# Performance work log

Measured on AMD Instinct MI355X. Metric: run time of the kernel, lower is better.

## Reference

```python
import jax, jax.numpy as jnp
import numpy as np

SEQ, BATCH, IN, HID, LAYERS, TAPE = 256, 128, 512, 512, 2, 30


def setup_inputs() -> dict:
    key = jax.random.key(0)
    ks = jax.random.split(key, 10)
    s = 0.05  # small init scale for numerical stability of tanh/softmax
    return {
        "xs": jax.random.normal(ks[0], (SEQ, BATCH, IN), jnp.float32),
        # stacked per-layer LSTM params (layer-1 input dim == HID == IN)
        "W_ih": jax.random.normal(ks[1], (LAYERS, 4 * HID, IN), jnp.float32) * s,
        "W_hh": jax.random.normal(ks[2], (LAYERS, 4 * HID, HID), jnp.float32) * s,
        "b_ih": jax.random.normal(ks[3], (LAYERS, 4 * HID), jnp.float32) * s,
        "b_hh": jax.random.normal(ks[4], (LAYERS, 4 * HID), jnp.float32) * s,
        "attn_wh": jax.random.normal(ks[5], (LAYERS, HID, HID), jnp.float32) * s,
        "attn_wx": jax.random.normal(ks[6], (LAYERS, HID, IN), jnp.float32) * s,
        "attn_wht": jax.random.normal(ks[7], (LAYERS, HID, HID), jnp.float32) * s,
        "attn_v": jax.random.normal(ks[8], (LAYERS, HID), jnp.float32) * s,
    }


def reference(xs, W_ih, W_hh, b_ih, b_hh, attn_wh, attn_wx, attn_wht, attn_v):
    L, B, H = W_ih.shape[0], xs.shape[1], W_hh.shape[-1]

    def lstm_step(x, h, c):
        # x: (B, IN); h, c: (L, B, H). PyTorch gate order: i, f, g, o.
        inp = x
        hs, cs = [], []
        for l in range(L):
            gates = inp @ W_ih[l].T + b_ih[l] + h[l] @ W_hh[l].T + b_hh[l]
            i_, f_, g_, o_ = jnp.split(gates, 4, axis=-1)
            c_new = jax.nn.sigmoid(f_) * c[l] + jax.nn.sigmoid(i_) * jnp.tanh(g_)
            h_new = jax.nn.sigmoid(o_) * jnp.tanh(c_new)
            hs.append(h_new)
            cs.append(c_new)
            inp = h_new
        return jnp.stack(hs), jnp.stack(cs)

    zeros = jnp.zeros((L, B, H), xs.dtype)
    # First TAPE steps: source never updates prev_hidden/cell inside the fill
    # loop, so every step starts from zero state -> vmap over time.
    h_tape0, c_tape0 = jax.vmap(lambda x: lstm_step(x, zeros, zeros))(xs[:TAPE])

    # einsums 'jll,...' / 'ijj,...' contract nothing: they take diagonals.
    wh_diag = jnp.diagonal(attn_wh, axis1=1, axis2=2)    # (L, H)
    wht_diag = jnp.diagonal(attn_wht, axis1=1, axis2=2)  # (L, H)

    def step(carry, x):
        h_tape, c_tape, prev_h = carry
        hidden_attn = h_tape * wh_diag[:, None, :]            # (T, L, B, H)
        x_attn = jnp.einsum('lhi,bi->lbh', attn_wx, x)        # (L, B, H)
        ht_attn = prev_h * wht_diag[:, None, :]               # (L, B, H)
        a = jnp.tanh(hidden_attn + x_attn + ht_attn)          # (T, L, B, H)
        score = jnp.einsum('tlbh,lh->tlb', a, attn_v)         # (T, L, B)
        alpha = jax.nn.softmax(score, axis=0)
        prev_h_new = jnp.einsum('tlb,tlbh->lbh', alpha, h_tape)
        prev_c_new = jnp.einsum('tlb,tlbh->lbh', alpha, c_tape)
        h_new, c_new = lstm_step(x, prev_h_new, prev_c_new)
        h_tape = jnp.concatenate([h_tape[1:], h_new[None]], axis=0)
        c_tape = jnp.concatenate([c_tape[1:], c_new[None]], axis=0)
        return (h_tape, c_tape, prev_h_new), None

    (h_tape, _, _), _ = jax.lax.scan(step, (h_tape0, c_tape0, zeros), xs[TAPE:])
    return h_tape[:, -1]  # (TAPE, B, H): last layer across the tape
```

## Files before the change

kernel.cpp:

```cpp
#include <hip/hip_runtime.h>
#include <hip/hip_fp16.h>

typedef _Float16 f16;
typedef _Float16 half8 __attribute__((ext_vector_type(8)));
typedef _Float16 half4v __attribute__((ext_vector_type(4)));
typedef float floatx4 __attribute__((ext_vector_type(4)));
typedef unsigned long long u64;

#define SEQ   256
#define BATCH 128
#define HID   512
#define NL    2
#define TAPE  30
#define NG    2048
#define NBLK  256

__device__ __forceinline__ float fsig(float x)  { return 1.f/(1.f+__expf(-x)); }
__device__ __forceinline__ float ftanh(float x) { return 1.f - 2.f/(1.f+__expf(2.f*x)); }

__device__ __forceinline__ void ast64(void* p, u64 v){
    __hip_atomic_store((u64*)p, v, __ATOMIC_RELAXED, __HIP_MEMORY_SCOPE_AGENT);
}
__device__ __forceinline__ void ast32(void* p, unsigned v){
    __hip_atomic_store((unsigned*)p, v, __ATOMIC_RELAXED, __HIP_MEMORY_SCOPE_AGENT);
}
__device__ __forceinline__ unsigned packh2(float a, float b){
    union { f16 h[2]; unsigned u; } c; c.h[0]=(f16)a; c.h[1]=(f16)b; return c.u;
}
__device__ __forceinline__ float2 unpackh2(unsigned u){
    union { unsigned u; f16 h[2]; } c; c.u=u;
    float2 r; r.x=(float)c.h[0]; r.y=(float)c.h[1]; return r;
}

#define BAR_ROOT 512
#define BAR_REL  544
__device__ __forceinline__ void gridbar(unsigned* bar, unsigned gen){
    __syncthreads();
    if (threadIdx.x == 0){
        unsigned* leaf = bar + ((blockIdx.x >> 4) << 5);
        bool releaser = false;
        unsigned p = __hip_atomic_fetch_add(leaf, 1u, __ATOMIC_RELAXED, __HIP_MEMORY_SCOPE_AGENT);
        if ((p & 15u) == 15u){
            unsigned q = __hip_atomic_fetch_add(bar + BAR_ROOT, 1u, __ATOMIC_RELAXED, __HIP_MEMORY_SCOPE_AGENT);
            if ((q & 15u) == 15u){
                __hip_atomic_store(bar + BAR_REL, gen, __ATOMIC_RELAXED, __HIP_MEMORY_SCOPE_AGENT);
                releaser = true;
            }
        }
        if (!releaser){
            while (__hip_atomic_load(bar + BAR_REL, __ATOMIC_RELAXED, __HIP_MEMORY_SCOPE_AGENT) < gen){
                __builtin_amdgcn_s_sleep(8);
            }
        }
        __builtin_amdgcn_fence(__ATOMIC_ACQUIRE, "agent");
    }
    __syncthreads();
}

__global__ void k_setup_w(const float* __restrict__ W_ih, const float* __restrict__ W_hh,
                          const float* __restrict__ b_ih, const float* __restrict__ b_hh,
                          f16* __restrict__ Wcat, float* __restrict__ bsum)
{
    int idx = blockIdx.x*256 + threadIdx.x;
    int l = idx >> 21;
    int r = (idx >> 10) & 2047;
    int k = idx & 1023;
    int gate = r & 3, h = r >> 2;
    int orig = gate*HID + h;
    float wv = (k < 512) ? W_ih[((size_t)l*NG + orig)*512 + k]
                         : W_hh[((size_t)l*NG + orig)*512 + (k-512)];
    Wcat[idx] = (f16)wv;
    if (idx < NL*NG) {
        int l2 = idx >> 11, r2 = idx & 2047;
        int g2 = r2 & 3, h2 = r2 >> 2;
        int o2 = g2*HID + h2;
        bsum[idx] = b_ih[l2*NG + o2] + b_hh[l2*NG + o2];
    }
}

__global__ void k_setup_misc(const float* __restrict__ attn_wx, const float* __restrict__ attn_wh,
                             const float* __restrict__ attn_wht, const float* __restrict__ attn_v,
                             f16* __restrict__ awx, float* __restrict__ whd,
                             float* __restrict__ whtd, float* __restrict__ av)
{
    int idx = blockIdx.x*256 + threadIdx.x;
    awx[idx] = (f16)attn_wx[idx];
    if (idx < NL*HID) {
        int l = idx >> 9, h = idx & 511;
        whd[idx]  = attn_wh[((size_t)l*HID + h)*HID + h];
        whtd[idx] = attn_wht[((size_t)l*HID + h)*HID + h];
        av[idx]   = attn_v[idx];
    }
}

__global__ void k_xs16(const float* __restrict__ x, f16* __restrict__ o)
{
    size_t i = ((size_t)blockIdx.x*256 + threadIdx.x)*4;
    float4 v = *(const float4*)(x + i);
    half4v h; h[0]=(f16)v.x; h[1]=(f16)v.y; h[2]=(f16)v.z; h[3]=(f16)v.w;
    *(half4v*)(o + i) = h;
}

#define MFMA4(af, bf) do { \
    acc[0][0] = __builtin_amdgcn_mfma_f32_16x16x32_f16(af[0], bf[0], acc[0][0], 0, 0, 0); \
    acc[0][1] = __builtin_amdgcn_mfma_f32_16x16x32_f16(af[0], bf[1], acc[0][1], 0, 0, 0); \
    acc[1][0] = __builtin_amdgcn_mfma_f32_16x16x32_f16(af[1], bf[0], acc[1][0], 0, 0, 0); \
    acc[1][1] = __builtin_amdgcn_mfma_f32_16x16x32_f16(af[1], bf[1], acc[1][1], 0, 0, 0); \
} while(0)

__global__ __launch_bounds__(512) void k_xattn(const f16* __restrict__ Xf,
                                               const f16* __restrict__ AWX,
                                               f16* __restrict__ XA)
{
    int nb = blockIdx.x;
    int t  = blockIdx.y;
    int l  = blockIdx.z;
    const f16* A  = Xf  + (size_t)t*(BATCH*512);
    const f16* Bm = AWX + (size_t)l*(512*512);
    int lane = threadIdx.x & 63, wid = threadIdx.x >> 6;
    int wm = wid >> 1, wn = wid & 1;
    int row0 = wm*32 + (lane & 15);
    int col0 = nb*64 + wn*32 + (lane & 15);
    int kc = (lane >> 4)*8;
    const f16* a_base = A  + row0*512 + kc;
    const f16* b_base = Bm + col0*512 + kc;
    floatx4 acc[2][2] = {};
    #pragma unroll 4
    for (int ks = 0; ks < 16; ks++){
        half8 af[2], bf[2];
        af[0] = *(const half8*)(a_base + ks*32);
        af[1] = *(const half8*)(a_base + 8192 + ks*32);
        bf[0] = *(const half8*)(b_base + ks*32);
        bf[1] = *(const half8*)(b_base + 8192 + ks*32);
        MFMA4(af, bf);
    }
    int rr = (lane >> 4)*4;
    #pragma unroll
    for (int mi = 0; mi < 2; mi++)
    #pragma unroll
    for (int ni = 0; ni < 2; ni++)
    #pragma unroll
    for (int j = 0; j < 4; j++){
        int brow = wm*32 + mi*16 + rr + j;
        int ch   = nb*64 + wn*32 + ni*16 + (lane & 15);
        XA[(((size_t)t*NL + l)*BATCH + brow)*HID + ch] = (f16)acc[mi][ni][j];
    }
}

__global__ __launch_bounds__(512) void k_fill(const f16* __restrict__ A0all,
                                              const f16* __restrict__ B,
                                              const float* __restrict__ bsum_l,
                                              f16* __restrict__ htape16, float* __restrict__ ctape,
                                              int l, f16* __restrict__ h0out)
{
    int y  = blockIdx.y;
    int nb = blockIdx.x;
    const f16* A0 = A0all + (size_t)y*(BATCH*HID);
    if (h0out) h0out += (size_t)y*(BATCH*HID);

    int tid = threadIdx.x, lane = tid & 63, wid = tid >> 6;
    int wm = wid >> 1, wn = wid & 1;
    int row0 = wm*32 + (lane & 15);
    int col0 = nb*64 + wn*32 + (lane & 15);
    int kc = (lane >> 4)*8;
    const f16* a_base = A0 + row0*512 + kc;
    const f16* b_base = B + (size_t)col0*1024 + kc;

    floatx4 acc[2][2] = {};
    #pragma unroll
    for (int ks = 0; ks < 16; ks++){
        half8 af[2], bf[2];
        af[0] = *(const half8*)(a_base + ks*32);
        af[1] = *(const half8*)(a_base + 16*512 + ks*32);
        bf[0] = *(const half8*)(b_base + ks*32);
        bf[1] = *(const half8*)(b_base + (size_t)16*1024 + ks*32);
        MFMA4(af, bf);
    }

    __shared__ float Cl[128][65];
    int rr = (lane >> 4)*4;
    #pragma unroll
    for (int mi = 0; mi < 2; mi++)
    #pragma unroll
    for (int ni = 0; ni < 2; ni++){
        float bias = bsum_l[col0 + ni*16];
        #pragma unroll
        for (int j = 0; j < 4; j++)
            Cl[wm*32 + mi*16 + rr + j][wn*32 + ni*16 + (lane & 15)] = acc[mi][ni][j] + bias;
    }
    __syncthreads();

    #pragma unroll
    for (int it = 0; it < 4; it++){
        int item = tid + it*512;
        int b = item >> 4, hl = item & 15;
        float gi = Cl[b][hl*4+0];
        float gg = Cl[b][hl*4+2];
        float go = Cl[b][hl*4+3];
        int hg = nb*16 + hl;
        float cn = fsig(gi)*ftanh(gg);
        float hn = fsig(go)*ftanh(cn);
        size_t toff = (((size_t)y*NL + l)*BATCH + b)*HID + hg;
        htape16[toff] = (f16)hn;
        ctape[toff]   = cn;
        if (h0out) h0out[b*HID + hg] = (f16)hn;
    }
}

struct SArgs {
    const f16* xsf; const f16* xattn; const f16* Wcat; const float* bsum;
    const float* whd; const float* whtd; const float* av;
    const f16* htape16; const float* ctape;
    float* prevc; f16* prevh16;
    f16* h016; float2* slotstage; float* out;
    unsigned* bar;
};

__global__ __launch_bounds__(256, 1) void k_scan(SArgs A)
{
    __shared__ f16 Wsh[16*1024];
    __shared__ float2 stg[128*4];
    __shared__ float wpart[TAPE][4];
    __shared__ unsigned ringH[TAPE][256];
    __shared__ unsigned ringC[TAPE][256];

    const int blk = blockIdx.x;
    const int tid = threadIdx.x;
    const int lane = tid & 63, wv = tid >> 6;
    const int myl = blk >> 7;
    const int cb  = blk & 127;
    const int b   = blk & 127;
    const int h0  = tid*2;
    const size_t BH = (size_t)BATCH*HID;

    {
        const f16* src = A.Wcat + ((size_t)myl*NG + (size_t)cb*16)*1024;
        for (int i = tid; i < 2048; i += 256){
            int c = i >> 7;
            int k = (i & 127)*8;
            int dst = (c << 10) | (k ^ ((c & 7) << 3));
            *(half8*)&Wsh[dst] = *(const half8*)(src + ((size_t)c << 10) + k);
        }
    }

    float phx = 0.f, phy = 0.f;
    #pragma unroll
    for (int p = 0; p < TAPE; p++){
        size_t off = (((size_t)p*NL + myl)*BATCH + b)*HID + h0;
        ringH[p][tid] = *(const unsigned*)(A.htape16 + off);
        float2 cc = *(const float2*)(A.ctape + off);
        ringC[p][tid] = packh2(cc.x, cc.y);
    }
    __syncthreads();

    auto do_attn = [&](int t, bool consume){
        if (consume){
            int snew = (t-1) % TAPE;
            const float2* sl2 = A.slotstage + ((size_t)myl*BATCH + b)*HID + h0;
            float2 c0 = sl2[0], c1 = sl2[1];
            ringH[snew][tid] = packh2(c0.x, c1.x);
            ringC[snew][tid] = packh2(c0.y, c1.y);
        }
        size_t pb = ((size_t)myl*BATCH + b)*HID + h0;
        unsigned xu = *(const unsigned*)(A.xattn + (((size_t)t*NL + myl)*BATCH + b)*HID + h0);
        float2 xa = unpackh2(xu);
        int hw = myl*HID + h0;
        float wdx = A.whd[hw],  wdy = A.whd[hw+1];
        float wtx = A.whtd[hw], wty = A.whtd[hw+1];
        float vvx = A.av[hw],   vvy = A.av[hw+1];
        float bx = xa.x + phx*wtx, by = xa.y + phy*wty;

        float sc[TAPE];
        #pragma unroll
        for (int p = 0; p < TAPE; p++){
            float2 hv = unpackh2(ringH[p][tid]);
            float ax = ftanh(hv.x*wdx + bx);
            float ay = ftanh(hv.y*wdy + by);
            float s = ax*vvx + ay*vvy;
            #pragma unroll
            for (int o = 32; o; o >>= 1) s += __shfl_xor(s, o);
            if (lane == 0) wpart[p][wv] = s;
        }
        __syncthreads();
        float m = -1e30f;
        #pragma unroll
        for (int p = 0; p < TAPE; p++){
            sc[p] = wpart[p][0] + wpart[p][1] + wpart[p][2] + wpart[p][3];
            m = fmaxf(m, sc[p]);
        }
        float Z = 0.f;
        #pragma unroll
        for (int p = 0; p < TAPE; p++){ sc[p] = __expf(sc[p] - m); Z += sc[p]; }
        float inv = 1.f/Z;
        float ahx=0.f, ahy=0.f, acx=0.f, acy=0.f;
        #pragma unroll
        for (int p = 0; p < TAPE; p++){
            float2 hv = unpackh2(ringH[p][tid]);
            float2 cv = unpackh2(ringC[p][tid]);
            ahx += sc[p]*hv.x; ahy += sc[p]*hv.y;
            acx += sc[p]*cv.x; acy += sc[p]*cv.y;
        }
        ahx*=inv; ahy*=inv; acx*=inv; acy*=inv;
        phx = ahx; phy = ahy;
        ast32(A.prevh16 + pb, packh2(ahx, ahy));
        union { float2 f; u64 u; } pc; pc.f.x = acx; pc.f.y = acy;
        ast64(A.prevc + pb, pc.u);
    };

    floatx4 acc0 = {0,0,0,0}, acc1 = {0,0,0,0};
    float cpv[2][4];
    const int colL = lane & 15;
    const int bofs = colL << 10;
    const int sw   = (colL & 7) << 3;
    const int rowT = wv*32;
    const int row0g = rowT + (lane & 15);
    const int kcl  = (lane >> 4)*8;
    const int rr   = (lane >> 4) << 2;
    const int hL   = colL >> 2;
    const int hG   = cb*4 + hL;

    auto load_cprev = [&](){
        const float* cprev_l = A.prevc + (size_t)myl*BH;
        #pragma unroll
        for (int mi = 0; mi < 2; mi++)
        #pragma unroll
        for (int j = 0; j < 4; j++)
            cpv[mi][j] = cprev_l[(size_t)(rowT + mi*16 + rr + j)*HID + hG];
    };

    auto gemm_half = [&](const f16* Abase, int kofs){
        const f16* a = Abase + (size_t)row0g*512 + kcl;
        half8 fa[16], fb[16];
        #pragma unroll
        for (int ks = 0; ks < 16; ks++){
            fa[ks] = *(const half8*)(a + ks*32);
            fb[ks] = *(const half8*)(a + ks*32 + 16*512);
        }
        #pragma unroll
        for (int ks = 0; ks < 16; ks++){
            int kx = (kcl + kofs + ks*32) ^ sw;
            half8 bf = *(const half8*)&Wsh[bofs + kx];
            acc0 = __builtin_amdgcn_mfma_f32_16x16x32_f16(fa[ks], bf, acc0, 0, 0, 0);
            acc1 = __builtin_amdgcn_mfma_f32_16x16x32_f16(fb[ks], bf, acc1, 0, 0, 0);
        }
    };

    auto gemm_fin = [&](f16* h0out, float* outp){
        int baseLane = lane & 60;
        float bias = A.bsum[myl*NG + cb*16 + colL];
        #pragma unroll
        for (int mi = 0; mi < 2; mi++){
            #pragma unroll
            for (int j = 0; j < 4; j++){
                float g = (mi ? acc1[j] : acc0[j]) + bias;
                float gi = __shfl(g, baseLane+0);
                float gf = __shfl(g, baseLane+1);
                float gg = __shfl(g, baseLane+2);
                float go = __shfl(g, baseLane+3);
                int row = rowT + mi*16 + rr + j;
                float cn = fsig(gf)*cpv[mi][j] + fsig(gi)*ftanh(gg);
                float hn = fsig(go)*ftanh(cn);
                if ((lane & 3) == 0){ float2 v; v.x=hn; v.y=cn; stg[row*4 + hL] = v; }
            }
        }
        __syncthreads();
        float2* slot2 = A.slotstage + (size_t)myl*BH;
        #pragma unroll
        for (int e = 0; e < 2; e++){
            int idx = tid + e*256;
            int row = idx >> 2, hh = idx & 3;
            union { float2 f; u64 u; } cu; cu.f = stg[idx];
            ast64(&slot2[(size_t)row*HID + cb*4 + hh], cu.u);
        }
        if (tid < 128){
            int row = tid;
            if (myl == 0){
                union { f16 h[4]; u64 u; } pk;
                pk.h[0]=(f16)stg[row*4+0].x; pk.h[1]=(f16)stg[row*4+1].x;
                pk.h[2]=(f16)stg[row*4+2].x; pk.h[3]=(f16)stg[row*4+3].x;
                ast64(h0out + (size_t)row*512 + cb*4, pk.u);
            } else {
                union { float2 f; u64 u; } p0, p1;
                p0.f.x = stg[row*4+0].x; p0.f.y = stg[row*4+1].x;
                p1.f.x = stg[row*4+2].x; p1.f.y = stg[row*4+3].x;
                ast64(outp + (size_t)row*512 + cb*4,     p0.u);
                ast64(outp + (size_t)row*512 + cb*4 + 2, p1.u);
            }
        }
        floatx4 z = {0,0,0,0};
        acc0 = z; acc1 = z;
    };

    if (myl == 0){
        do_attn(TAPE, false);
        gemm_half(A.xsf + (size_t)TAPE*BH, 0);
    }
    unsigned gen = 0;
    gridbar(A.bar, ++gen);

    for (int t = TAPE; t < SEQ; ++t){
        if (myl == 0){
            load_cprev();
            gemm_half(A.prevh16, 512);
            gemm_fin(A.h016, nullptr);
        } else if (t > TAPE){
            load_cprev();
            gemm_half(A.prevh16 + BH, 512);
            gemm_fin(nullptr, A.out + (size_t)((t-1-16) % TAPE)*BH);
        }
        gridbar(A.bar, ++gen);
        if (myl == 0){
            if (t + 1 < SEQ){
                do_attn(t + 1, true);
                gemm_half(A.xsf + (size_t)(t+1)*BH, 0);
            }
        } else {
            do_attn(t, t > TAPE);
            gemm_half(A.h016, 0);
        }
        gridbar(A.bar, ++gen);
    }
    if (myl == 1){
        load_cprev();
        gemm_half(A.prevh16 + BH, 512);
        gemm_fin(nullptr, A.out + (size_t)((SEQ-1-16) % TAPE)*BH);
    }
}

extern "C" void kernel_launch(void* const* d_in, const int* in_sizes, int n_in,
                              void* d_out, int out_size, void* d_ws, size_t ws_size,
                              hipStream_t stream)
{
    (void)in_sizes; (void)n_in; (void)out_size; (void)ws_size;
    const float* xs       = (const float*)d_in[0];
    const float* W_ih     = (const float*)d_in[1];
    const float* W_hh     = (const float*)d_in[2];
    const float* b_ih     = (const float*)d_in[3];
    const float* b_hh     = (const float*)d_in[4];
    const float* attn_wh  = (const float*)d_in[5];
    const float* attn_wx  = (const float*)d_in[6];
    const float* attn_wht = (const float*)d_in[7];
    const float* attn_v   = (const float*)d_in[8];
    float* out = (float*)d_out;

    char* w = (char*)d_ws;
    auto alloc = [&](size_t bytes)->char*{ char* p = w; w += (bytes + 255) & ~(size_t)255; return p; };
    f16*   Wcat    = (f16*)   alloc((size_t)NL*NG*1024*2);
    float* bsum    = (float*) alloc((size_t)NL*NG*4);
    f16*   awx     = (f16*)   alloc((size_t)NL*HID*HID*2);
    float* whd     = (float*) alloc((size_t)NL*HID*4);
    float* whtd    = (float*) alloc((size_t)NL*HID*4);
    float* av      = (float*) alloc((size_t)NL*HID*4);
    f16*   xsf     = (f16*)   alloc((size_t)SEQ*BATCH*HID*2);
    f16*   xattn   = (f16*)   alloc((size_t)SEQ*NL*BATCH*HID*2);
    f16*   htape16 = (f16*)   alloc((size_t)TAPE*NL*BATCH*HID*2);
    float* ctape   = (float*) alloc((size_t)TAPE*NL*BATCH*HID*4);
    float* prevc   = (float*) alloc((size_t)NL*BATCH*HID*4);
    f16*   prevh16 = (f16*)   alloc((size_t)NL*BATCH*HID*2);
    f16*   h016    = (f16*)   alloc((size_t)BATCH*HID*2);
    f16*   h0all   = (f16*)   alloc((size_t)TAPE*BATCH*HID*2);
    float2* slotstage = (float2*)alloc((size_t)NL*BATCH*HID*8);
    unsigned* bar  = (unsigned*)alloc(4096);

    hipMemsetAsync(prevc,   0, (size_t)NL*BATCH*HID*4, stream);
    hipMemsetAsync(prevh16, 0, (size_t)NL*BATCH*HID*2, stream);
    hipMemsetAsync(bar,     0, 4096, stream);

    k_setup_w   <<<dim3(16384), dim3(256), 0, stream>>>(W_ih, W_hh, b_ih, b_hh, Wcat, bsum);
    k_setup_misc<<<dim3(2048),  dim3(256), 0, stream>>>(attn_wx, attn_wh, attn_wht, attn_v, awx, whd, whtd, av);
    k_xs16      <<<dim3(16384), dim3(256), 0, stream>>>(xs, xsf);
    k_xattn     <<<dim3(8, SEQ, NL), dim3(512), 0, stream>>>(xsf, awx, xattn);

    k_fill<<<dim3(32, TAPE), dim3(512), 0, stream>>>(xsf, Wcat, bsum, htape16, ctape, 0, h0all);
    k_fill<<<dim3(32, TAPE), dim3(512), 0, stream>>>(h0all, Wcat + (size_t)NG*1024, bsum + NG,
                                                     htape16, ctape, 1, nullptr);

    SArgs sa;
    sa.xsf = xsf; sa.xattn = xattn; sa.Wcat = Wcat; sa.bsum = bsum;
    sa.whd = whd; sa.whtd = whtd; sa.av = av;
    sa.htape16 = htape16; sa.ctape = ctape;
    sa.prevc = prevc; sa.prevh16 = prevh16;
    sa.h016 = h016; sa.slotstage = slotstage; sa.out = out;
    sa.bar = bar;
    k_scan<<<dim3(NBLK), dim3(256), 0, stream>>>(sa);
}
```

Baseline: 7.158 ms.

## Split grid barrier into arrive/wait and overlap attention scoring with barrier latency

The grid barrier is split into separate arrive and wait phases. Between them, each block scores the attention tape entries that do not depend on the newly produced slot. After the wait, only the newest slot is scored before the softmax, and the input-side GEMM half is moved after the second arrive. The aim is to hide barrier latency on the serial recurrence behind independent work. The spin-wait sleep interval is also shortened, which polls more often and adds more atomic load traffic.

```diff
diff --git a/kernel.cpp b/kernel.cpp
--- a/kernel.cpp
+++ b/kernel.cpp
@@ -34,23 +34,23 @@
 
 #define BAR_ROOT 512
 #define BAR_REL  544
-__device__ __forceinline__ void gridbar(unsigned* bar, unsigned gen){
+__device__ __forceinline__ void bar_arrive(unsigned* bar, unsigned gen){
     __syncthreads();
     if (threadIdx.x == 0){
         unsigned* leaf = bar + ((blockIdx.x >> 4) << 5);
-        bool releaser = false;
         unsigned p = __hip_atomic_fetch_add(leaf, 1u, __ATOMIC_RELAXED, __HIP_MEMORY_SCOPE_AGENT);
         if ((p & 15u) == 15u){
             unsigned q = __hip_atomic_fetch_add(bar + BAR_ROOT, 1u, __ATOMIC_RELAXED, __HIP_MEMORY_SCOPE_AGENT);
             if ((q & 15u) == 15u){
                 __hip_atomic_store(bar + BAR_REL, gen, __ATOMIC_RELAXED, __HIP_MEMORY_SCOPE_AGENT);
-                releaser = true;
             }
         }
-        if (!releaser){
-            while (__hip_atomic_load(bar + BAR_REL, __ATOMIC_RELAXED, __HIP_MEMORY_SCOPE_AGENT) < gen){
-                __builtin_amdgcn_s_sleep(8);
-            }
+    }
+}
+__device__ __forceinline__ void bar_wait(unsigned* bar, unsigned gen){
+    if (threadIdx.x == 0){
+        while (__hip_atomic_load(bar + BAR_REL, __ATOMIC_RELAXED, __HIP_MEMORY_SCOPE_AGENT) < gen){
+            __builtin_amdgcn_s_sleep(2);
         }
         __builtin_amdgcn_fence(__ATOMIC_ACQUIRE, "agent");
     }
@@ -253,36 +253,50 @@
     }
     __syncthreads();
 
-    auto do_attn = [&](int t, bool consume){
-        if (consume){
-            int snew = (t-1) % TAPE;
-            const float2* sl2 = A.slotstage + ((size_t)myl*BATCH + b)*HID + h0;
-            float2 c0 = sl2[0], c1 = sl2[1];
-            ringH[snew][tid] = packh2(c0.x, c1.x);
-            ringC[snew][tid] = packh2(c0.y, c1.y);
-        }
-        size_t pb = ((size_t)myl*BATCH + b)*HID + h0;
+    float p_wdx, p_wdy, p_vvx, p_vvy, p_bx, p_by;
+
+    auto attn_pre = [&](int t, int snew){
         unsigned xu = *(const unsigned*)(A.xattn + (((size_t)t*NL + myl)*BATCH + b)*HID + h0);
         float2 xa = unpackh2(xu);
         int hw = myl*HID + h0;
-        float wdx = A.whd[hw],  wdy = A.whd[hw+1];
+        p_wdx = A.whd[hw];  p_wdy = A.whd[hw+1];
         float wtx = A.whtd[hw], wty = A.whtd[hw+1];
-        float vvx = A.av[hw],   vvy = A.av[hw+1];
-        float bx = xa.x + phx*wtx, by = xa.y + phy*wty;
-
-        float sc[TAPE];
+        p_vvx = A.av[hw];   p_vvy = A.av[hw+1];
+        p_bx = xa.x + phx*wtx;
+        p_by = xa.y + phy*wty;
         #pragma unroll
         for (int p = 0; p < TAPE; p++){
-            float2 hv = unpackh2(ringH[p][tid]);
-            float ax = ftanh(hv.x*wdx + bx);
-            float ay = ftanh(hv.y*wdy + by);
-            float s = ax*vvx + ay*vvy;
+            if (p != snew){
+                float2 hv = unpackh2(ringH[p][tid]);
+                float ax = ftanh(hv.x*p_wdx + p_bx);
+                float ay = ftanh(hv.y*p_wdy + p_by);
+                float s = ax*p_vvx + ay*p_vvy;
+                #pragma unroll
+                for (int o = 32; o; o >>= 1) s += __shfl_xor(s, o);
+                if (lane == 0) wpart[p][wv] = s;
+            }
+        }
+    };
+
+    auto attn_post = [&](int snew){
+        size_t pb = ((size_t)myl*BATCH + b)*HID + h0;
+        if (snew >= 0){
+            const float2* sl2 = A.slotstage + ((size_t)myl*BATCH + b)*HID + h0;
+            float2 c0 = sl2[0], c1 = sl2[1];
+            unsigned nh = packh2(c0.x, c1.x);
+            unsigned nc = packh2(c0.y, c1.y);
+            ringH[snew][tid] = nh;
+            ringC[snew][tid] = nc;
+            float2 hv = unpackh2(nh);
+            float ax = ftanh(hv.x*p_wdx + p_bx);
+            float ay = ftanh(hv.y*p_wdy + p_by);
+            float s = ax*p_vvx + ay*p_vvy;
             #pragma unroll
             for (int o = 32; o; o >>= 1) s += __shfl_xor(s, o);
-            if (lane == 0) wpart[p][wv] = s;
+            if (lane == 0) wpart[snew][wv] = s;
         }
         __syncthreads();
-        float m = -1e30f;
+        float sc[TAPE]; float m = -1e30f;
         #pragma unroll
         for (int p = 0; p < TAPE; p++){
             sc[p] = wpart[p][0] + wpart[p][1] + wpart[p][2] + wpart[p][3];
@@ -391,34 +405,41 @@
         acc0 = z; acc1 = z;
     };
 
+    unsigned gen = 0;
     if (myl == 0){
-        do_attn(TAPE, false);
+        attn_pre(TAPE, -1);
+        attn_post(-1);
         gemm_half(A.xsf + (size_t)TAPE*BH, 0);
     }
-    unsigned gen = 0;
-    gridbar(A.bar, ++gen);
+    ++gen; bar_arrive(A.bar, gen); bar_wait(A.bar, gen);
 
     for (int t = TAPE; t < SEQ; ++t){
         if (myl == 0){
             load_cprev();
             gemm_half(A.prevh16, 512);
             gemm_fin(A.h016, nullptr);
-        } else if (t > TAPE){
-            load_cprev();
-            gemm_half(A.prevh16 + BH, 512);
-            gemm_fin(nullptr, A.out + (size_t)((t-1-16) % TAPE)*BH);
-        }
-        gridbar(A.bar, ++gen);
+            ++gen; bar_arrive(A.bar, gen);
+            if (t + 1 < SEQ) attn_pre(t + 1, t % TAPE);
+        } else {
+            if (t > TAPE){
+                load_cprev();
+                gemm_half(A.prevh16 + BH, 512);
+                gemm_fin(nullptr, A.out + (size_t)((t-1-16) % TAPE)*BH);
+            }
+            ++gen; bar_arrive(A.bar, gen);
+            attn_pre(t, t > TAPE ? (t-1) % TAPE : -1);
+        }
+        bar_wait(A.bar, gen);
         if (myl == 0){
-            if (t + 1 < SEQ){
-                do_attn(t + 1, true);
-                gemm_half(A.xsf + (size_t)(t+1)*BH, 0);
-            }
+            if (t + 1 < SEQ) attn_post(t % TAPE);
+            ++gen; bar_arrive(A.bar, gen);
+            if (t + 1 < SEQ) gemm_half(A.xsf + (size_t)(t+1)*BH, 0);
         } else {
-            do_attn(t, t > TAPE);
+            attn_post(t > TAPE ? (t-1) % TAPE : -1);
+            ++gen; bar_arrive(A.bar, gen);
             gemm_half(A.h016, 0);
         }
-        gridbar(A.bar, ++gen);
+        bar_wait(A.bar, gen);
     }
     if (myl == 1){
         load_cprev();
```

After: 6.420 ms, median of 2. 10.3% less time.
